# Optimization experiments

Hardware: AMD Instinct MI355X
Metric: run time of the kernel (lower is better)

Reference implementation:

```python
import jax, jax.numpy as jnp
import numpy as np
from itertools import product

N = 200000      # occupied fine voxels
G = 256         # grid extent per axis
C0, C1 = 32, 64 # nPlanes
EPS = 1e-4      # BatchNormBlock eps


def _enc(p):
    return (p[:, 0].astype(np.int64) * G + p[:, 1]) * G + p[:, 2]


def _lookup(q, keys):
    # keys: sorted encoded positions; returns index into position array, sentinel=len(keys) if absent
    n = keys.shape[0]
    valid = ((q >= 0) & (q < G)).all(1)
    qe = _enc(np.clip(q, 0, G - 1))
    i = np.searchsorted(keys, qe)
    ic = np.clip(i, 0, n - 1)
    found = valid & (keys[ic] == qe)
    return np.where(found, ic, n).astype(np.int32)


def _build_geometry():
    rng = np.random.default_rng(0)
    lin = np.sort(rng.choice(G ** 3, size=N, replace=False))
    pos = np.stack(np.unravel_index(lin, (G, G, G)), -1).astype(np.int64)  # [N,3], enc(pos)==lin sorted
    keys = lin
    off27 = np.array(list(product((-1, 0, 1), repeat=3)), dtype=np.int64)
    nbr_fine = np.stack([_lookup(pos + o, keys) for o in off27])  # [27,N]
    # Convolution.calculate_grid: even positions among pos+{-1,0}^3, min>=0, unique, then /2
    f8 = np.array(list(product((-1, 0), repeat=3)), dtype=np.int64)
    cand = (pos[:, None, :] + f8[None]).reshape(-1, 3)
    cand = cand[cand.min(1) >= 0]
    cand = cand[(cand % 2 == 0).all(1)]
    cand = np.unique(cand, axis=0)
    cpos = cand // 2                       # [M,3] coarse coords
    ckeys = _enc(cpos)                     # lexsorted rows -> sorted keys
    off2 = np.array([[(i >> 2) & 1, (i >> 1) & 1, i & 1] for i in range(8)], dtype=np.int64)
    down_idx = np.stack([_lookup(2 * cpos + o, keys) for o in off2])  # [8,M] into fine feats

    def _lookup_c(q):
        n = ckeys.shape[0]
        valid = ((q >= 0) & (q < G)).all(1)
        qe = _enc(np.clip(q, 0, G - 1))
        i = np.searchsorted(ckeys, qe)
        ic = np.clip(i, 0, n - 1)
        found = valid & (ckeys[ic] == qe)
        return np.where(found, ic, n).astype(np.int32)

    nbr_coarse = np.stack([_lookup_c(cpos + o) for o in off27])  # [27,M]
    up_cidx = _lookup_c(pos // 2)  # [N], always found (coverage guaranteed by calculate_grid)
    up_k = ((pos[:, 0] % 2) * 4 + (pos[:, 1] % 2) * 2 + (pos[:, 2] % 2)).astype(np.int32)
    return nbr_fine, nbr_coarse, down_idx, up_cidx, up_k


def setup_inputs() -> dict:
    nbr_fine, nbr_coarse, down_idx, up_cidx, up_k = _build_geometry()
    key = jax.random.key(0)
    ks = jax.random.split(key, 8)

    def w(k, shape, fan_in):
        return jax.random.normal(k, shape, jnp.float32) * (1.0 / np.sqrt(fan_in))

    return dict(
        feat=jax.random.normal(ks[0], (N, C0), jnp.float32),
        w_sub1=w(ks[1], (27, C0, C0), 27 * C0),
        w_down=w(ks[2], (8, C0, C1), 8 * C0),
        w_sub2=w(ks[3], (27, C1, C1), 27 * C1),
        w_up=w(ks[4], (8, C1, C0), 8 * C1),
        w_sub3=w(ks[5], (27, 2 * C0, C0), 27 * 2 * C0),
        g1=jnp.ones(C0), b1=jnp.zeros(C0),
        g2=jnp.ones(C0), b2=jnp.zeros(C0),
        g3=jnp.ones(C1), b3=jnp.zeros(C1),
        g4=jnp.ones(C1), b4=jnp.zeros(C1),
        g5=jnp.ones(2 * C0), b5=jnp.zeros(2 * C0),
        nbr_fine=jnp.asarray(nbr_fine), nbr_coarse=jnp.asarray(nbr_coarse),
        down_idx=jnp.asarray(down_idx), up_cidx=jnp.asarray(up_cidx),
        up_k=jnp.asarray(up_k),
    )


def _bn_relu(x, g, b):
    # BatchNormBlock (training-mode batch stats over concatenated voxels) + ReLUBlock
    mu = x.mean(0)
    var = x.var(0)
    return jax.nn.relu(g * (x - mu) * jax.lax.rsqrt(var + EPS) + b)


def _sparse_conv(feat, nbr, W):
    # gather-GEMM-accumulate: feat [P,Cin], nbr [K,M] (sentinel P -> zero), W [K,Cin,Cout]
    fpad = jnp.concatenate([feat, jnp.zeros((1, feat.shape[1]), feat.dtype)], 0)

    def body(acc, kw):
        idx, w = kw
        return acc + fpad[idx] @ w, None

    acc0 = jnp.zeros((nbr.shape[1], W.shape[2]), feat.dtype)
    out, _ = jax.lax.scan(body, acc0, (nbr, W))
    return out


def _sparse_deconv(cfeat, up_cidx, up_k, W):
    # stride-2 transpose conv: each fine voxel reads its unique coarse parent with kernel tap up_k
    g = cfeat[up_cidx]  # [N,Cin]
    out = jnp.zeros((g.shape[0], W.shape[2]), cfeat.dtype)
    for k in range(8):
        out = out + jnp.where(up_k == k, 1.0, 0.0)[:, None] * (g @ W[k])
    return out


def reference(feat, w_sub1, w_down, w_sub2, w_up, w_sub3,
              g1, b1, g2, b2, g3, b3, g4, b4, g5, b5,
              nbr_fine, nbr_coarse, down_idx, up_cidx, up_k):
    # block(32->32): BN -> ReLU -> SubmanifoldSparseConv 3x3x3
    x = _sparse_conv(_bn_relu(feat, g1, b1), nbr_fine, w_sub1)
    skip = x  # ConcatFeat
    # BN -> ReLU -> Convolution 2x2x2 (downsample 32->64)
    xc = _sparse_conv(_bn_relu(x, g2, b2), down_idx, w_down)
    # inner level block(64->64)
    xc = _sparse_conv(_bn_relu(xc, g3, b3), nbr_coarse, w_sub2)
    # BN -> ReLU -> DeConvolution 2x2x2 (upsample 64->32)
    xf = _sparse_deconv(_bn_relu(xc, g4, b4), up_cidx, up_k, w_up)
    # JoinFeat: concat(skip, upsampled)
    x = jnp.concatenate([skip, xf], -1)
    # block(64->32)
    x = _sparse_conv(_bn_relu(x, g5, b5), nbr_fine, w_sub3)
    return x
```

## Files before the change

### kernel.cpp

```cpp
#include <hip/hip_runtime.h>


#define EPS 1e-4f

typedef __attribute__((ext_vector_type(8))) short short8;
typedef __attribute__((ext_vector_type(4))) float f32x4;

__device__ __forceinline__ unsigned short f2bf(float f) {
    union { float f; unsigned int u; } v; v.f = f;
    unsigned int r = v.u + 0x7fffu + ((v.u >> 16) & 1u);
    return (unsigned short)(r >> 16);
}

__global__ void zero_kernel(float* p, long n) {
    long i = (long)blockIdx.x * 256 + threadIdx.x;
    if (i < n) p[i] = 0.f;
}

template <int C>
__global__ __launch_bounds__(256) void bn_stats(const float* __restrict__ x,
                                                int rows, int stride,
                                                float* __restrict__ stats) {
    const int tid = threadIdx.x;
    const int c = tid & (C - 1);
    const int g = tid / C;
    const int GR = 256 / C;
    float s = 0.f, s2 = 0.f;
    for (int r = blockIdx.x * GR + g; r < rows; r += gridDim.x * GR) {
        float v = x[(size_t)r * stride + c];
        s += v; s2 += v * v;
    }
    __shared__ float sh[2][256];
    sh[0][tid] = s; sh[1][tid] = s2;
    __syncthreads();
    for (int off = 128; off >= C; off >>= 1) {
        if (tid < off) { sh[0][tid] += sh[0][tid + off]; sh[1][tid] += sh[1][tid + off]; }
        __syncthreads();
    }
    if (tid < C) {
        atomicAdd(&stats[c], sh[0][tid]);
        atomicAdd(&stats[C + c], sh[1][tid]);
    }
}

template <int C, int CSPLIT>
__global__ __launch_bounds__(256) void bn_norm_relu_bf16(
    const float* __restrict__ x, int rows, int stride,
    const float* __restrict__ stA, const float* __restrict__ stB,
    const float* __restrict__ gamma, const float* __restrict__ beta,
    unsigned short* __restrict__ y) {
    constexpr int TPR = C / 8;
    int gid = blockIdx.x * 256 + threadIdx.x;
    int r = gid / TPR, t = gid % TPR;
    if (r > rows) return;
    short8 o8;
    if (r == rows) {
        for (int j = 0; j < 8; ++j) o8[j] = 0;
    } else {
        const float inv_n = 1.0f / (float)rows;
        const float* xr = x + (size_t)r * stride + t * 8;
        float4 v0 = *(const float4*)(xr);
        float4 v1 = *(const float4*)(xr + 4);
        float vv[8] = {v0.x, v0.y, v0.z, v0.w, v1.x, v1.y, v1.z, v1.w};
#pragma unroll
        for (int j = 0; j < 8; ++j) {
            int c = t * 8 + j;
            const float* st = (c < CSPLIT) ? stA : stB;
            int cc = (c < CSPLIT) ? c : c - CSPLIT;
            int cs = (c < CSPLIT) ? CSPLIT : (C - CSPLIT);
            float mu = st[cc] * inv_n;
            float var = st[cs + cc] * inv_n - mu * mu;
            float sc = gamma[c] * rsqrtf(var + EPS);
            float shf = beta[c] - mu * sc;
            float ov = fmaxf(0.f, fmaf(vv[j], sc, shf));
            o8[j] = (short)f2bf(ov);
        }
    }
    *(short8*)(y + (size_t)r * C + t * 8) = o8;
}

__device__ __forceinline__ void wt_seg(const float* W, unsigned short* WT,
                                       int id, int CIN, int COUT) {
    int r = id % (CIN * COUT);
    int t = id / (CIN * COUT);
    int co = r / CIN;
    int ci = r % CIN;
    WT[id] = f2bf(W[(size_t)t * CIN * COUT + ci * COUT + co]);
}
__global__ __launch_bounds__(256) void wt_transpose_all(
    const float* w1, const float* wd, const float* w2, const float* w3,
    const float* wu, unsigned short* o1, unsigned short* od,
    unsigned short* o2, unsigned short* o3, unsigned short* ou) {
    int id = blockIdx.x * 256 + threadIdx.x;
    if (id < 27648) { wt_seg(w1, o1, id, 32, 32); return; }
    id -= 27648;
    if (id < 16384) { wt_seg(wd, od, id, 32, 64); return; }
    id -= 16384;
    if (id < 110592) { wt_seg(w2, o2, id, 64, 64); return; }
    id -= 110592;
    if (id < 55296) { wt_seg(w3, o3, id, 64, 32); return; }
    id -= 55296;
    if (id < 16384) { wt_seg(wu, ou, id, 64, 32); return; }
}

__global__ __launch_bounds__(256) void build_rb_up(
    const int* __restrict__ up_cidx, const int* __restrict__ up_k,
    int rows, int cap, int2* __restrict__ rb, int* __restrict__ cnt) {
    const int s = blockIdx.y;
    const int lane = threadIdx.x & 63;
    const int wave = threadIdx.x >> 6;
    const long wbase = (long)blockIdx.x * 1024 + wave * 256;

    unsigned long long masks[4];
    int cs[4], ok[4], tot[4], wtotal = 0;
#pragma unroll
    for (int c = 0; c < 4; ++c) {
        long i = wbase + c * 64 + lane;
        int seg = (i < rows) ? up_k[i] : -1;
        cs[c] = (i < rows) ? up_cidx[i] : 0;
        ok[c] = (seg == s);
        masks[c] = __ballot(ok[c]);
        tot[c] = __popcll(masks[c]);
        wtotal += tot[c];
    }
    __shared__ int sh[5];
    if (lane == 0) sh[wave] = wtotal;
    __syncthreads();
    if (threadIdx.x == 0) {
        int t = sh[0] + sh[1] + sh[2] + sh[3];
        sh[4] = t ? atomicAdd(&cnt[s * 32], t) : 0;
    }
    __syncthreads();
    int base = sh[4];
    for (int w = 0; w < wave; ++w) base += sh[w];
#pragma unroll
    for (int c = 0; c < 4; ++c) {
        if (ok[c]) {
            int rank = __popcll(masks[c] & ((1ull << lane) - 1ull));
            int j = base + rank;
            if (j < cap)
                rb[(size_t)s * cap + j] = make_int2((int)(wbase + c * 64 + lane), cs[c]);
        }
        base += tot[c];
    }
}


template <int CIN, int COT, int NTAP, int MT>
__global__ __launch_bounds__(256) void conv_dense(
    const unsigned short* __restrict__ fpad,
    const int* __restrict__ nbr,
    const unsigned short* __restrict__ WT,
    float* __restrict__ out,
    float* __restrict__ stats,
    int rows, int P, int out_stride) {
    constexpr int N_SUB = COT / 16;
    constexpr int K_SUB = CIN / 32;
    const int tid = threadIdx.x;
    const int wave = tid >> 6;
    const int lane = tid & 63;
    const int q = lane >> 4;
    const int l15 = lane & 15;
    const int m0 = blockIdx.x * (64 * MT) + wave * (16 * MT);

    int mrow[MT], mok[MT];
#pragma unroll
    for (int mt = 0; mt < MT; ++mt) {
        int m = m0 + mt * 16 + l15;
        mok[mt] = (m < rows);
        mrow[mt] = mok[mt] ? m : 0;
    }

    f32x4 acc[MT][N_SUB];
#pragma unroll
    for (int mt = 0; mt < MT; ++mt)
#pragma unroll
        for (int nt = 0; nt < N_SUB; ++nt) acc[mt][nt] = (f32x4){0.f, 0.f, 0.f, 0.f};

    int idx[MT];
#pragma unroll
    for (int mt = 0; mt < MT; ++mt)
        idx[mt] = mok[mt] ? nbr[mrow[mt]] : P;

    for (int k = 0; k < NTAP; ++k) {
        int nxt[MT];
#pragma unroll
        for (int mt = 0; mt < MT; ++mt)
            nxt[mt] = (k + 1 < NTAP && mok[mt]) ? nbr[(size_t)(k + 1) * rows + mrow[mt]] : P;

        const unsigned short* Wk = WT + (size_t)k * COT * CIN;
        short8 b[N_SUB][K_SUB];
#pragma unroll
        for (int nt = 0; nt < N_SUB; ++nt)
#pragma unroll
            for (int kf = 0; kf < K_SUB; ++kf)
                b[nt][kf] = *(const short8*)(Wk + (size_t)(nt * 16 + l15) * CIN + kf * 32 + q * 8);

        short8 a[MT][K_SUB];
#pragma unroll
        for (int mt = 0; mt < MT; ++mt) {
            const unsigned short* ap = fpad + (size_t)idx[mt] * CIN + q * 8;
#pragma unroll
            for (int kf = 0; kf < K_SUB; ++kf)
                a[mt][kf] = *(const short8*)(ap + kf * 32);
        }
#pragma unroll
        for (int mt = 0; mt < MT; ++mt)
#pragma unroll
            for (int nt = 0; nt < N_SUB; ++nt)
#pragma unroll
                for (int kf = 0; kf < K_SUB; ++kf)
                    acc[mt][nt] = __builtin_amdgcn_mfma_f32_16x16x32_bf16(
                        a[mt][kf], b[nt][kf], acc[mt][nt], 0, 0, 0);
#pragma unroll
        for (int mt = 0; mt < MT; ++mt) idx[mt] = nxt[mt];
    }

#pragma unroll
    for (int mt = 0; mt < MT; ++mt)
#pragma unroll
        for (int i = 0; i < 4; ++i) {
            int row = m0 + mt * 16 + q * 4 + i;
            if (row < rows) {
#pragma unroll
                for (int nt = 0; nt < N_SUB; ++nt)
                    out[(size_t)row * out_stride + nt * 16 + l15] = acc[mt][nt][i];
            }
        }

    if (stats) {
        __shared__ float ssum[COT], ssq[COT];
        for (int i = tid; i < 2 * COT; i += 256)
            (i < COT ? ssum[i] : ssq[i - COT]) = 0.f;
        __syncthreads();
#pragma unroll
        for (int nt = 0; nt < N_SUB; ++nt) {
            float s = 0.f, s2 = 0.f;
#pragma unroll
            for (int mt = 0; mt < MT; ++mt)
#pragma unroll
                for (int i = 0; i < 4; ++i) {
                    float v = acc[mt][nt][i];
                    s += v; s2 += v * v;
                }
            s += __shfl_xor(s, 16);  s += __shfl_xor(s, 32);
            s2 += __shfl_xor(s2, 16); s2 += __shfl_xor(s2, 32);
            if (q == 0) {
                atomicAdd(&ssum[nt * 16 + l15], s);
                atomicAdd(&ssq[nt * 16 + l15], s2);
            }
        }
        __syncthreads();
        if (tid < COT) {
            atomicAdd(&stats[tid], ssum[tid]);
            atomicAdd(&stats[COT + tid], ssq[tid]);
        }
    }
}

template <int CIN, int COT, bool ATOMIC>
__global__ __launch_bounds__(256) void conv_sparse(
    const unsigned short* __restrict__ fpad,
    const int2* __restrict__ rb,
    const int* __restrict__ cnt,
    const unsigned short* __restrict__ WT,
    float* __restrict__ out,
    float* __restrict__ stats,
    int cap, int kskip, int P, int out_stride) {
    constexpr int N_SUB = COT / 16;
    constexpr int K_SUB = CIN / 32;
    const int tap = blockIdx.y;
    int n = cnt[tap * 32];
    n = n < cap ? n : cap;
    const int nbx = gridDim.x;
    const int step = (nbx >> 3) | 1;
    const int px = (int)((blockIdx.x + (unsigned)tap * step) % (unsigned)nbx);
    const int base0 = px * 128;
    if (base0 >= n) return;
    const int k = tap + (tap >= kskip ? 1 : 0);
    const int tid = threadIdx.x;
    const int wave = tid >> 6;
    const int lane = tid & 63;
    const int q = lane >> 4;
    const int l15 = lane & 15;
    const int base = base0 + wave * 32;
    const int2* seg = rb + (size_t)tap * cap;

    f32x4 acc[2][N_SUB];
#pragma unroll
    for (int mt = 0; mt < 2; ++mt)
#pragma unroll
        for (int nt = 0; nt < N_SUB; ++nt) acc[mt][nt] = (f32x4){0.f, 0.f, 0.f, 0.f};

    short8 a[2][K_SUB], b[N_SUB][K_SUB];
#pragma unroll
    for (int mt = 0; mt < 2; ++mt) {
        int j = base + mt * 16 + l15;
        int src = (j < n) ? seg[j].y : P;
#pragma unroll
        for (int kf = 0; kf < K_SUB; ++kf)
            a[mt][kf] = *(const short8*)(fpad + (size_t)src * CIN + kf * 32 + q * 8);
    }
    const unsigned short* Wk = WT + (size_t)k * COT * CIN;
#pragma unroll
    for (int nt = 0; nt < N_SUB; ++nt)
#pragma unroll
        for (int kf = 0; kf < K_SUB; ++kf)
            b[nt][kf] = *(const short8*)(Wk + (size_t)(nt * 16 + l15) * CIN + kf * 32 + q * 8);
#pragma unroll
    for (int mt = 0; mt < 2; ++mt)
#pragma unroll
        for (int nt = 0; nt < N_SUB; ++nt)
#pragma unroll
            for (int kf = 0; kf < K_SUB; ++kf)
                acc[mt][nt] = __builtin_amdgcn_mfma_f32_16x16x32_bf16(
                    a[mt][kf], b[nt][kf], acc[mt][nt], 0, 0, 0);

#pragma unroll
    for (int mt = 0; mt < 2; ++mt)
#pragma unroll
        for (int i = 0; i < 4; ++i) {
            int j = base + mt * 16 + q * 4 + i;
            if (j < n) {
                int row = seg[j].x;
                float* o = out + (size_t)row * out_stride + l15;
#pragma unroll
                for (int nt = 0; nt < N_SUB; ++nt) {
                    if (ATOMIC) atomicAdd(o + nt * 16, acc[mt][nt][i]);
                    else        o[nt * 16] = acc[mt][nt][i];
                }
            }
        }

    if (!ATOMIC && stats) {
        __shared__ float ssum[COT], ssq[COT];
        for (int i = tid; i < 2 * COT; i += 256)
            (i < COT ? ssum[i] : ssq[i - COT]) = 0.f;
        __syncthreads();
#pragma unroll
        for (int nt = 0; nt < N_SUB; ++nt) {
            float s = 0.f, s2 = 0.f;
#pragma unroll
            for (int mt = 0; mt < 2; ++mt)
#pragma unroll
                for (int i = 0; i < 4; ++i) {
                    float v = acc[mt][nt][i];
                    s += v; s2 += v * v;
                }
            s += __shfl_xor(s, 16);  s += __shfl_xor(s, 32);
            s2 += __shfl_xor(s2, 16); s2 += __shfl_xor(s2, 32);
            if (q == 0) {
                atomicAdd(&ssum[nt * 16 + l15], s);
                atomicAdd(&ssq[nt * 16 + l15], s2);
            }
        }
        __syncthreads();
        if (tid < COT) {
            atomicAdd(&stats[tid], ssum[tid]);
            atomicAdd(&stats[COT + tid], ssq[tid]);
        }
    }
}

static inline int ceil_div(long a, long b) { return (int)((a + b - 1) / b); }

extern "C" void kernel_launch(void* const* d_in, const int* in_sizes, int n_in,
                              void* d_out, int out_size, void* d_ws, size_t ws_size,
                              hipStream_t stream) {
    const float* feat   = (const float*)d_in[0];
    const float* w_sub1 = (const float*)d_in[1];
    const float* w_down = (const float*)d_in[2];
    const float* w_sub2 = (const float*)d_in[3];
    const float* w_up   = (const float*)d_in[4];
    const float* w_sub3 = (const float*)d_in[5];
    const float* g1 = (const float*)d_in[6],  *b1 = (const float*)d_in[7];
    const float* g2 = (const float*)d_in[8],  *b2 = (const float*)d_in[9];
    const float* g3 = (const float*)d_in[10], *b3 = (const float*)d_in[11];
    const float* g4 = (const float*)d_in[12], *b4 = (const float*)d_in[13];
    const float* g5 = (const float*)d_in[14], *b5 = (const float*)d_in[15];
    const int* nbr_fine   = (const int*)d_in[16];
    const int* nbr_coarse = (const int*)d_in[17];
    const int* down_idx   = (const int*)d_in[18];
    const int* up_cidx    = (const int*)d_in[19];
    const int* up_k       = (const int*)d_in[20];

    const int N = in_sizes[0] / 32;
    const int M = in_sizes[17] / 27;
    const size_t maxr = (size_t)((N > M ? N : M) + 1);

    const int cap_u = 32768;

    char* ws = (char*)d_ws;
    size_t off = 0;
    auto alloc = [&](size_t bytes) { void* p = ws + off; off += (bytes + 255) & ~(size_t)255; return p; };
    float* stats = (float*)alloc(768 * sizeof(float));
    int*   cnts  = (int*)alloc(1024 * sizeof(int));
    const size_t zero_words = off / 4;
    float* D  = (float*)alloc((size_t)N * 64 * sizeof(float));
    float* Cf = (float*)alloc((size_t)M * 64 * sizeof(float));
    unsigned short* FA = (unsigned short*)alloc(maxr * 64 * 2);
    unsigned short* FB = (unsigned short*)alloc(maxr * 64 * 2);
    int2* rb_up = (int2*)alloc((size_t)8 * cap_u * sizeof(int2));
    unsigned short* w1t = (unsigned short*)alloc(27 * 32 * 32 * 2);
    unsigned short* wdt = (unsigned short*)alloc(8 * 32 * 64 * 2);
    unsigned short* w2t = (unsigned short*)alloc(27 * 64 * 64 * 2);
    unsigned short* w3t = (unsigned short*)alloc(27 * 64 * 32 * 2);
    unsigned short* wupT = (unsigned short*)alloc(8 * 64 * 32 * 2);

    float* st0 = stats + 0 * 128;
    float* st1 = stats + 1 * 128;
    float* st2 = stats + 2 * 128;
    float* st3 = stats + 3 * 128;
    float* st4 = stats + 4 * 128;
    int* cnt_up = cnts;

    zero_kernel<<<ceil_div((long)zero_words, 256), 256, 0, stream>>>(stats, (long)zero_words);
    wt_transpose_all<<<ceil_div(226304, 256), 256, 0, stream>>>(
        w_sub1, w_down, w_sub2, w_sub3, w_up, w1t, wdt, w2t, w3t, wupT);
    build_rb_up<<<dim3(ceil_div(N, 1024), 8), 256, 0, stream>>>(
        up_cidx, up_k, N, cap_u, rb_up, cnt_up);

    bn_stats<32><<<256, 256, 0, stream>>>(feat, N, 32, st0);
    bn_norm_relu_bf16<32, 32><<<ceil_div((long)(N + 1) * 4, 256), 256, 0, stream>>>(
        feat, N, 32, st0, st0, g1, b1, FA);
    conv_dense<32, 32, 27, 2><<<ceil_div(N, 128), 256, 0, stream>>>(
        FA, nbr_fine, w1t, D, st1, N, N, 64);
    bn_norm_relu_bf16<32, 32><<<ceil_div((long)(N + 1) * 4, 256), 256, 0, stream>>>(
        D, N, 64, st1, st1, g2, b2, FB);
    conv_dense<32, 64, 8, 4><<<ceil_div(M, 256), 256, 0, stream>>>(
        FB, down_idx, wdt, Cf, st2, M, N, 64);
    bn_norm_relu_bf16<64, 64><<<ceil_div((long)(M + 1) * 8, 256), 256, 0, stream>>>(
        Cf, M, 64, st2, st2, g3, b3, FA);
    conv_dense<64, 64, 27, 4><<<ceil_div(M, 256), 256, 0, stream>>>(
        FA, nbr_coarse, w2t, Cf, st3, M, M, 64);
    bn_norm_relu_bf16<64, 64><<<ceil_div((long)(M + 1) * 8, 256), 256, 0, stream>>>(
        Cf, M, 64, st3, st3, g4, b4, FB);
    conv_sparse<64, 32, false><<<dim3(cap_u / 128, 8), 256, 0, stream>>>(
        FB, rb_up, cnt_up, wupT, D + 32, st4, cap_u, 99, M, 64);
    bn_norm_relu_bf16<64, 32><<<ceil_div((long)(N + 1) * 8, 256), 256, 0, stream>>>(
        D, N, 64, st1, st4, g5, b5, FA);
    conv_dense<64, 32, 27, 4><<<ceil_div(N, 256), 256, 0, stream>>>(
        FA, nbr_fine, w3t, (float*)d_out, nullptr, N, N, 32);
}
```

Before: 618.2 us.

## Software-pipeline neighbor gathers against MFMA in the dense sparse-conv kernel

Restructures the conv_dense tap loop so the gathered A fragments are split into two halves, each in its own register buffer. While one half runs its MFMAs, the next tap's gather for the other half is issued, along with the weights and neighbor indices one tap further ahead. The aim is to hide the latency of the irregular feature gathers behind matrix work. In exchange the tap loop is fully unrolled and more registers stay live, which can lower occupancy and enlarge the code. The split assumes MT is even.

```diff
diff --git a/kernel.cpp b/kernel.cpp
--- a/kernel.cpp
+++ b/kernel.cpp
@@ -156,6 +156,7 @@
     int rows, int P, int out_stride) {
     constexpr int N_SUB = COT / 16;
     constexpr int K_SUB = CIN / 32;
+    constexpr int MH = MT / 2;
     const int tid = threadIdx.x;
     const int wave = tid >> 6;
     const int lane = tid & 63;
@@ -177,43 +178,69 @@
 #pragma unroll
         for (int nt = 0; nt < N_SUB; ++nt) acc[mt][nt] = (f32x4){0.f, 0.f, 0.f, 0.f};
 
-    int idx[MT];
-#pragma unroll
-    for (int mt = 0; mt < MT; ++mt)
-        idx[mt] = mok[mt] ? nbr[mrow[mt]] : P;
-
-    for (int k = 0; k < NTAP; ++k) {
-        int nxt[MT];
+    short8 aLo[MH][K_SUB], aHi[MH][K_SUB];
+    short8 b[N_SUB][K_SUB];
+    int idxN[MT];
+
+    auto load_idx = [&](int k) {
 #pragma unroll
         for (int mt = 0; mt < MT; ++mt)
-            nxt[mt] = (k + 1 < NTAP && mok[mt]) ? nbr[(size_t)(k + 1) * rows + mrow[mt]] : P;
-
+            idxN[mt] = mok[mt] ? nbr[(size_t)k * rows + mrow[mt]] : P;
+    };
+    auto gather_half = [&](short8 (&a)[MH][K_SUB], int hoff) {
+#pragma unroll
+        for (int h = 0; h < MH; ++h) {
+            const unsigned short* ap = fpad + (size_t)idxN[hoff + h] * CIN + q * 8;
+#pragma unroll
+            for (int kf = 0; kf < K_SUB; ++kf)
+                a[h][kf] = *(const short8*)(ap + kf * 32);
+        }
+    };
+    auto gather_half0 = [&](short8 (&a)[MH][K_SUB], int hoff, int k0) {
+#pragma unroll
+        for (int h = 0; h < MH; ++h) {
+            int idx = mok[hoff + h] ? nbr[(size_t)k0 * rows + mrow[hoff + h]] : P;
+            const unsigned short* ap = fpad + (size_t)idx * CIN + q * 8;
+#pragma unroll
+            for (int kf = 0; kf < K_SUB; ++kf)
+                a[h][kf] = *(const short8*)(ap + kf * 32);
+        }
+    };
+    auto load_b = [&](int k) {
         const unsigned short* Wk = WT + (size_t)k * COT * CIN;
-        short8 b[N_SUB][K_SUB];
 #pragma unroll
         for (int nt = 0; nt < N_SUB; ++nt)
 #pragma unroll
             for (int kf = 0; kf < K_SUB; ++kf)
                 b[nt][kf] = *(const short8*)(Wk + (size_t)(nt * 16 + l15) * CIN + kf * 32 + q * 8);
-
-        short8 a[MT][K_SUB];
-#pragma unroll
-        for (int mt = 0; mt < MT; ++mt) {
-            const unsigned short* ap = fpad + (size_t)idx[mt] * CIN + q * 8;
-#pragma unroll
-            for (int kf = 0; kf < K_SUB; ++kf)
-                a[mt][kf] = *(const short8*)(ap + kf * 32);
-        }
-#pragma unroll
-        for (int mt = 0; mt < MT; ++mt)
+    };
+    auto mfma_half = [&](short8 (&a)[MH][K_SUB], int hoff) {
+#pragma unroll
+        for (int h = 0; h < MH; ++h)
 #pragma unroll
             for (int nt = 0; nt < N_SUB; ++nt)
 #pragma unroll
                 for (int kf = 0; kf < K_SUB; ++kf)
-                    acc[mt][nt] = __builtin_amdgcn_mfma_f32_16x16x32_bf16(
-                        a[mt][kf], b[nt][kf], acc[mt][nt], 0, 0, 0);
-#pragma unroll
-        for (int mt = 0; mt < MT; ++mt) idx[mt] = nxt[mt];
+                    acc[hoff + h][nt] = __builtin_amdgcn_mfma_f32_16x16x32_bf16(
+                        a[h][kf], b[nt][kf], acc[hoff + h][nt], 0, 0, 0);
+    };
+
+    gather_half0(aLo, 0, 0);
+    gather_half0(aHi, MH, 0);
+    load_b(0);
+    if (NTAP > 1) load_idx(1);
+
+#pragma unroll
+    for (int k = 0; k < NTAP; ++k) {
+        const bool more = (k + 1 < NTAP);
+        mfma_half(aLo, 0);
+        if (more) gather_half(aLo, 0);
+        mfma_half(aHi, MH);
+        if (more) {
+            load_b(k + 1);
+            gather_half(aHi, MH);
+            if (k + 2 < NTAP) load_idx(k + 2);
+        }
     }
 
 #pragma unroll
```

Result: no change. 607.0 us (-1.8%).

## Stage conv weights into LDS with async loads and double-buffer feature gathers

Applied to the files above, without the earlier changes.

Weights are pre-permuted into MFMA fragment order so each lane reads a contiguous 16-byte chunk. The dense conv kernel stages each tap's weights into double-buffered LDS with global_load_lds, and ping-pongs the gathered feature fragments so tap k+1's loads overlap tap k's MFMAs. Per-block row tiles drop from MT=4 to MT=2 to offset the extra register and LDS pressure. The cost is a __syncthreads per tap and a fully unrolled tap loop that may grow code size and register use.

```diff
diff --git a/kernel.cpp b/kernel.cpp
--- a/kernel.cpp
+++ b/kernel.cpp
@@ -85,7 +85,13 @@
     int t = id / (CIN * COUT);
     int co = r / CIN;
     int ci = r % CIN;
-    WT[id] = f2bf(W[(size_t)t * CIN * COUT + ci * COUT + co]);
+    int ksub = CIN >> 5;
+    int nt = co >> 4, l15 = co & 15;
+    int kf = (ksub > 1) ? (ci >> 5) : 0;
+    int qq = (ci >> 3) & 3;
+    int e  = ci & 7;
+    int off = ((nt * ksub + kf) * 64 + (qq * 16 + l15)) * 8 + e;
+    WT[(size_t)t * CIN * COUT + off] = f2bf(W[(size_t)t * CIN * COUT + ci * COUT + co]);
 }
 __global__ __launch_bounds__(256) void wt_transpose_all(
     const float* w1, const float* wd, const float* w2, const float* w3,
@@ -156,6 +162,9 @@
     int rows, int P, int out_stride) {
     constexpr int N_SUB = COT / 16;
     constexpr int K_SUB = CIN / 32;
+    constexpr int TAP_SH = COT * CIN;
+    constexpr int TOT_I = TAP_SH / 512;
+    __shared__ unsigned short ldsB[2][TAP_SH];
     const int tid = threadIdx.x;
     const int wave = tid >> 6;
     const int lane = tid & 63;
@@ -177,33 +186,41 @@
 #pragma unroll
         for (int nt = 0; nt < N_SUB; ++nt) acc[mt][nt] = (f32x4){0.f, 0.f, 0.f, 0.f};
 
-    int idx[MT];
-#pragma unroll
-    for (int mt = 0; mt < MT; ++mt)
-        idx[mt] = mok[mt] ? nbr[mrow[mt]] : P;
-
-    for (int k = 0; k < NTAP; ++k) {
-        int nxt[MT];
+    short8 aA[MT][K_SUB], aB[MT][K_SUB];
+    short8 b[N_SUB][K_SUB];
+    int idxC[MT];
+
+    auto stage_b = [&](int k, int buf) {
+        const unsigned short* src = WT + (size_t)k * TAP_SH;
+        for (int j = wave; j < TOT_I; j += 4) {
+            __builtin_amdgcn_global_load_lds(
+                (const __attribute__((address_space(1))) void*)(src + j * 512 + lane * 8),
+                (__attribute__((address_space(3))) void*)(&ldsB[buf][j * 512]),
+                16, 0, 0);
+        }
+    };
+    auto load_b_lds = [&](int buf) {
+#pragma unroll
+        for (int nt = 0; nt < N_SUB; ++nt)
+#pragma unroll
+            for (int kf = 0; kf < K_SUB; ++kf)
+                b[nt][kf] = *(const short8*)(&ldsB[buf][((nt * K_SUB + kf) * 64 + lane) * 8]);
+    };
+    auto load_idx = [&](int k) {
 #pragma unroll
         for (int mt = 0; mt < MT; ++mt)
-            nxt[mt] = (k + 1 < NTAP && mok[mt]) ? nbr[(size_t)(k + 1) * rows + mrow[mt]] : P;
-
-        const unsigned short* Wk = WT + (size_t)k * COT * CIN;
-        short8 b[N_SUB][K_SUB];
-#pragma unroll
-        for (int nt = 0; nt < N_SUB; ++nt)
-#pragma unroll
-            for (int kf = 0; kf < K_SUB; ++kf)
-                b[nt][kf] = *(const short8*)(Wk + (size_t)(nt * 16 + l15) * CIN + kf * 32 + q * 8);
-
-        short8 a[MT][K_SUB];
+            idxC[mt] = mok[mt] ? nbr[(size_t)k * rows + mrow[mt]] : P;
+    };
+    auto gather = [&](short8 (&a)[MT][K_SUB]) {
 #pragma unroll
         for (int mt = 0; mt < MT; ++mt) {
-            const unsigned short* ap = fpad + (size_t)idx[mt] * CIN + q * 8;
+            const unsigned short* ap = fpad + (size_t)idxC[mt] * CIN + q * 8;
 #pragma unroll
             for (int kf = 0; kf < K_SUB; ++kf)
                 a[mt][kf] = *(const short8*)(ap + kf * 32);
         }
+    };
+    auto do_mfma = [&](short8 (&a)[MT][K_SUB]) {
 #pragma unroll
         for (int mt = 0; mt < MT; ++mt)
 #pragma unroll
@@ -212,8 +229,25 @@
                 for (int kf = 0; kf < K_SUB; ++kf)
                     acc[mt][nt] = __builtin_amdgcn_mfma_f32_16x16x32_bf16(
                         a[mt][kf], b[nt][kf], acc[mt][nt], 0, 0, 0);
-#pragma unroll
-        for (int mt = 0; mt < MT; ++mt) idx[mt] = nxt[mt];
+    };
+
+    stage_b(0, 0);
+    load_idx(0);
+    gather(aA);
+    if (NTAP > 1) load_idx(1);
+    __syncthreads();
+
+#pragma unroll
+    for (int k = 0; k < NTAP; ++k) {
+        const int cur = k & 1;
+        load_b_lds(cur);
+        if (k + 1 < NTAP) {
+            stage_b(k + 1, cur ^ 1);
+            if (k & 1) gather(aA); else gather(aB);
+            if (k + 2 < NTAP) load_idx(k + 2);
+        }
+        if (k & 1) do_mfma(aB); else do_mfma(aA);
+        if (k + 1 < NTAP) __syncthreads();
     }
 
 #pragma unroll
@@ -306,7 +340,7 @@
     for (int nt = 0; nt < N_SUB; ++nt)
 #pragma unroll
         for (int kf = 0; kf < K_SUB; ++kf)
-            b[nt][kf] = *(const short8*)(Wk + (size_t)(nt * 16 + l15) * CIN + kf * 32 + q * 8);
+            b[nt][kf] = *(const short8*)(Wk + ((nt * K_SUB + kf) * 64 + lane) * 8);
 #pragma unroll
     for (int mt = 0; mt < 2; ++mt)
 #pragma unroll
@@ -427,11 +461,11 @@
         FA, nbr_fine, w1t, D, st1, N, N, 64);
     bn_norm_relu_bf16<32, 32><<<ceil_div((long)(N + 1) * 4, 256), 256, 0, stream>>>(
         D, N, 64, st1, st1, g2, b2, FB);
-    conv_dense<32, 64, 8, 4><<<ceil_div(M, 256), 256, 0, stream>>>(
+    conv_dense<32, 64, 8, 2><<<ceil_div(M, 128), 256, 0, stream>>>(
         FB, down_idx, wdt, Cf, st2, M, N, 64);
     bn_norm_relu_bf16<64, 64><<<ceil_div((long)(M + 1) * 8, 256), 256, 0, stream>>>(
         Cf, M, 64, st2, st2, g3, b3, FA);
-    conv_dense<64, 64, 27, 4><<<ceil_div(M, 256), 256, 0, stream>>>(
+    conv_dense<64, 64, 27, 2><<<ceil_div(M, 128), 256, 0, stream>>>(
         FA, nbr_coarse, w2t, Cf, st3, M, M, 64);
     bn_norm_relu_bf16<64, 64><<<ceil_div((long)(M + 1) * 8, 256), 256, 0, stream>>>(
         Cf, M, 64, st3, st3, g4, b4, FB);
@@ -439,6 +473,6 @@
         FB, rb_up, cnt_up, wupT, D + 32, st4, cap_u, 99, M, 64);
     bn_norm_relu_bf16<64, 32><<<ceil_div((long)(N + 1) * 8, 256), 256, 0, stream>>>(
         D, N, 64, st1, st4, g5, b5, FA);
-    conv_dense<64, 32, 27, 4><<<ceil_div(N, 256), 256, 0, stream>>>(
+    conv_dense<64, 32, 27, 2><<<ceil_div(N, 128), 256, 0, stream>>>(
         FA, nbr_fine, w3t, (float*)d_out, nullptr, N, N, 32);
 }
```

Measured after the change: 540.9 us. 1.14x faster.
